# Performance work log

Measured on AMD Instinct MI355X. Metric: run time of the kernel, lower is better.

Reference implementation:

```python
import jax, jax.numpy as jnp
import numpy as np


def setup_inputs() -> dict:
    key = jax.random.key(0)
    k1, k2 = jax.random.split(key)
    L, B, H = 1024, 64, 1024
    encoder_outputs = jax.random.normal(k1, (L, B, H), dtype=jnp.float32)
    decoder_gru_out = jax.random.normal(k2, (1, B, H), dtype=jnp.float32)
    return {"encoder_outputs": encoder_outputs, "decoder_gru_out": decoder_gru_out}


def reference(encoder_outputs, decoder_gru_out):
    # scores[l,b] = sum_h enc[l,b,h] * dec[0,b,h]
    scores = jnp.einsum('lbh,bh->lb', encoder_outputs, decoder_gru_out[0])
    # softmax over the sequence (L) axis
    attn = jax.nn.softmax(scores, axis=0)  # [L, B]
    # context[b,h] = sum_l attn[l,b] * enc[l,b,h]
    context = jnp.einsum('lb,lbh->bh', attn, encoder_outputs)
    return context
```

## Files before the change

kernel.cpp:

```cpp
#include <hip/hip_runtime.h>
#include <math.h>

#define L_SEQ 1024
#define BATCH 64
#define HDIM  1024
#define WPB   4

__global__ __launch_bounds__(256) void attn_partial_kernel(
    const float* __restrict__ enc, const float* __restrict__ dec,
    float* __restrict__ wsC, float* __restrict__ wsML,
    int split, int chunk)
{
    const int tid  = threadIdx.x;
    const int lane = tid & 63;
    const int wave = tid >> 6;
    const int w    = blockIdx.x * WPB + wave;
    const int b    = w / split;
    const int k    = w - b * split;
    const int l0   = k * chunk;

    const float4* decv = (const float4*)(dec + (size_t)b * HDIM);
    const float4 d0 = decv[lane];
    const float4 d1 = decv[lane + 64];
    const float4 d2 = decv[lane + 128];
    const float4 d3 = decv[lane + 192];

    float m = -INFINITY;
    float lsum = 0.0f;
    float4 a0 = make_float4(0.f, 0.f, 0.f, 0.f);
    float4 a1 = a0, a2 = a0, a3 = a0;

    for (int l = l0; l < l0 + chunk; ++l) {
        const float4* row = (const float4*)(enc + ((size_t)l * BATCH + b) * HDIM);
        const float4 e0 = row[lane];
        const float4 e1 = row[lane + 64];
        const float4 e2 = row[lane + 128];
        const float4 e3 = row[lane + 192];

        float p = e0.x * d0.x + e0.y * d0.y + e0.z * d0.z + e0.w * d0.w;
        p += e1.x * d1.x + e1.y * d1.y + e1.z * d1.z + e1.w * d1.w;
        p += e2.x * d2.x + e2.y * d2.y + e2.z * d2.z + e2.w * d2.w;
        p += e3.x * d3.x + e3.y * d3.y + e3.z * d3.z + e3.w * d3.w;

        #pragma unroll
        for (int off = 32; off > 0; off >>= 1)
            p += __shfl_xor(p, off, 64);

        const float mn    = fmaxf(m, p);
        const float scale = __expf(m - mn);
        const float pe    = __expf(p - mn);
        m = mn;
        lsum = lsum * scale + pe;
        a0.x = a0.x * scale + pe * e0.x;  a0.y = a0.y * scale + pe * e0.y;
        a0.z = a0.z * scale + pe * e0.z;  a0.w = a0.w * scale + pe * e0.w;
        a1.x = a1.x * scale + pe * e1.x;  a1.y = a1.y * scale + pe * e1.y;
        a1.z = a1.z * scale + pe * e1.z;  a1.w = a1.w * scale + pe * e1.w;
        a2.x = a2.x * scale + pe * e2.x;  a2.y = a2.y * scale + pe * e2.y;
        a2.z = a2.z * scale + pe * e2.z;  a2.w = a2.w * scale + pe * e2.w;
        a3.x = a3.x * scale + pe * e3.x;  a3.y = a3.y * scale + pe * e3.y;
        a3.z = a3.z * scale + pe * e3.z;  a3.w = a3.w * scale + pe * e3.w;
    }

    const size_t r = (size_t)b * split + k;
    float4* C = (float4*)(wsC + r * (size_t)HDIM);
    C[lane]       = a0;
    C[lane + 64]  = a1;
    C[lane + 128] = a2;
    C[lane + 192] = a3;
    if (lane == 0) {
        wsML[2 * r]     = m;
        wsML[2 * r + 1] = lsum;
    }
}

__global__ __launch_bounds__(256) void attn_reduce_kernel(
    const float* __restrict__ wsC, const float* __restrict__ wsML,
    float* __restrict__ out, int split)
{
    const int b = blockIdx.x;
    const int t = threadIdx.x;

    float M = -INFINITY;
    for (int k = 0; k < split; ++k)
        M = fmaxf(M, wsML[2 * ((size_t)b * split + k)]);

    float Ltot = 0.0f;
    float4 acc = make_float4(0.f, 0.f, 0.f, 0.f);
    for (int k = 0; k < split; ++k) {
        const size_t r = (size_t)b * split + k;
        const float wgt = __expf(wsML[2 * r] - M);
        Ltot += wsML[2 * r + 1] * wgt;
        const float4 c = ((const float4*)(wsC + r * (size_t)HDIM))[t];
        acc.x += c.x * wgt;  acc.y += c.y * wgt;
        acc.z += c.z * wgt;  acc.w += c.w * wgt;
    }
    const float inv = 1.0f / Ltot;
    float4 o;
    o.x = acc.x * inv;  o.y = acc.y * inv;
    o.z = acc.z * inv;  o.w = acc.w * inv;
    ((float4*)(out + (size_t)b * HDIM))[t] = o;
}

extern "C" void kernel_launch(void* const* d_in, const int* in_sizes, int n_in,
                              void* d_out, int out_size, void* d_ws, size_t ws_size,
                              hipStream_t stream) {
    const float* enc = (const float*)d_in[0];
    const float* dec = (const float*)d_in[1];
    float* out = (float*)d_out;

    int split = 32;
    while (split > 1) {
        const size_t need = (size_t)BATCH * split * HDIM * sizeof(float)
                          + (size_t)BATCH * split * 2 * sizeof(float);
        if (need <= ws_size) break;
        split >>= 1;
    }
    const int chunk = L_SEQ / split;

    float* wsC  = (float*)d_ws;
    float* wsML = wsC + (size_t)BATCH * split * HDIM;

    const int nblocks = (BATCH * split) / WPB;
    attn_partial_kernel<<<nblocks, 256, 0, stream>>>(enc, dec, wsC, wsML, split, chunk);
    attn_reduce_kernel<<<BATCH, 256, 0, stream>>>(wsC, wsML, out, split);
}
```

Measured before the change: 367.4 us.

## Process four sequence rows per iteration, use exp2 softmax, widen split and reduce grid

The partial kernel now loads four encoder rows per iteration, so more memory loads are in flight, and it batches the shuffle reductions and the online-softmax rescale, with one rescale per group of four rows. Scores are converted to base-2 so exp2f can replace __expf. The split count rises from 32 to 64 when the workspace allows, and the reduce kernel uses four times as many blocks with scalar loads. The cost is much higher register use from the 16 float4 row values, which can lower occupancy, plus a larger workspace write and read.

```diff
diff --git a/kernel.cpp b/kernel.cpp
--- a/kernel.cpp
+++ b/kernel.cpp
@@ -5,6 +5,8 @@
 #define BATCH 64
 #define HDIM  1024
 #define WPB   4
+
+#define LOG2E 1.44269504088896340736f
 
 __global__ __launch_bounds__(256) void attn_partial_kernel(
     const float* __restrict__ enc, const float* __restrict__ dec,
@@ -20,53 +22,75 @@
     const int l0   = k * chunk;
 
     const float4* decv = (const float4*)(dec + (size_t)b * HDIM);
-    const float4 d0 = decv[lane];
-    const float4 d1 = decv[lane + 64];
-    const float4 d2 = decv[lane + 128];
-    const float4 d3 = decv[lane + 192];
+    float4 d[4];
+    #pragma unroll
+    for (int q = 0; q < 4; ++q) d[q] = decv[lane + 64 * q];
 
     float m = -INFINITY;
     float lsum = 0.0f;
-    float4 a0 = make_float4(0.f, 0.f, 0.f, 0.f);
-    float4 a1 = a0, a2 = a0, a3 = a0;
+    float4 a[4];
+    #pragma unroll
+    for (int q = 0; q < 4; ++q) a[q] = make_float4(0.f, 0.f, 0.f, 0.f);
 
-    for (int l = l0; l < l0 + chunk; ++l) {
-        const float4* row = (const float4*)(enc + ((size_t)l * BATCH + b) * HDIM);
-        const float4 e0 = row[lane];
-        const float4 e1 = row[lane + 64];
-        const float4 e2 = row[lane + 128];
-        const float4 e3 = row[lane + 192];
+    const size_t row_stride = (size_t)BATCH * HDIM;
 
-        float p = e0.x * d0.x + e0.y * d0.y + e0.z * d0.z + e0.w * d0.w;
-        p += e1.x * d1.x + e1.y * d1.y + e1.z * d1.z + e1.w * d1.w;
-        p += e2.x * d2.x + e2.y * d2.y + e2.z * d2.z + e2.w * d2.w;
-        p += e3.x * d3.x + e3.y * d3.y + e3.z * d3.z + e3.w * d3.w;
+    for (int g = 0; g < chunk; g += 4) {
+        const float* base = enc + ((size_t)(l0 + g) * BATCH + b) * HDIM;
+
+        float4 e[4][4];
+        #pragma unroll
+        for (int r = 0; r < 4; ++r) {
+            const float4* row = (const float4*)(base + r * row_stride);
+            #pragma unroll
+            for (int q = 0; q < 4; ++q) e[r][q] = row[lane + 64 * q];
+        }
+
+        float p[4];
+        #pragma unroll
+        for (int r = 0; r < 4; ++r) {
+            float s = 0.0f;
+            #pragma unroll
+            for (int q = 0; q < 4; ++q) {
+                s = fmaf(e[r][q].x, d[q].x, s);
+                s = fmaf(e[r][q].y, d[q].y, s);
+                s = fmaf(e[r][q].z, d[q].z, s);
+                s = fmaf(e[r][q].w, d[q].w, s);
+            }
+            p[r] = s;
+        }
 
         #pragma unroll
-        for (int off = 32; off > 0; off >>= 1)
-            p += __shfl_xor(p, off, 64);
+        for (int off = 32; off > 0; off >>= 1) {
+            p[0] += __shfl_xor(p[0], off, 64);
+            p[1] += __shfl_xor(p[1], off, 64);
+            p[2] += __shfl_xor(p[2], off, 64);
+            p[3] += __shfl_xor(p[3], off, 64);
+        }
 
-        const float mn    = fmaxf(m, p);
-        const float scale = __expf(m - mn);
-        const float pe    = __expf(p - mn);
+        const float s0 = p[0] * LOG2E, s1 = p[1] * LOG2E;
+        const float s2 = p[2] * LOG2E, s3 = p[3] * LOG2E;
+        const float mn = fmaxf(m, fmaxf(fmaxf(s0, s1), fmaxf(s2, s3)));
+        const float scale = exp2f(m - mn);
+        const float w0 = exp2f(s0 - mn);
+        const float w1 = exp2f(s1 - mn);
+        const float w2 = exp2f(s2 - mn);
+        const float w3 = exp2f(s3 - mn);
         m = mn;
-        lsum = lsum * scale + pe;
-        a0.x = a0.x * scale + pe * e0.x;  a0.y = a0.y * scale + pe * e0.y;
-        a0.z = a0.z * scale + pe * e0.z;  a0.w = a0.w * scale + pe * e0.w;
-        a1.x = a1.x * scale + pe * e1.x;  a1.y = a1.y * scale + pe * e1.y;
-        a1.z = a1.z * scale + pe * e1.z;  a1.w = a1.w * scale + pe * e1.w;
-        a2.x = a2.x * scale + pe * e2.x;  a2.y = a2.y * scale + pe * e2.y;
-        a2.z = a2.z * scale + pe * e2.z;  a2.w = a2.w * scale + pe * e2.w;
-        a3.x = a3.x * scale + pe * e3.x;  a3.y = a3.y * scale + pe * e3.y;
-        a3.z = a3.z * scale + pe * e3.z;  a3.w = a3.w * scale + pe * e3.w;
+        lsum = fmaf(lsum, scale, (w0 + w1) + (w2 + w3));
+
+        #pragma unroll
+        for (int q = 0; q < 4; ++q) {
+            a[q].x = fmaf(w3, e[3][q].x, fmaf(w2, e[2][q].x, fmaf(w1, e[1][q].x, fmaf(w0, e[0][q].x, a[q].x * scale))));
+            a[q].y = fmaf(w3, e[3][q].y, fmaf(w2, e[2][q].y, fmaf(w1, e[1][q].y, fmaf(w0, e[0][q].y, a[q].y * scale))));
+            a[q].z = fmaf(w3, e[3][q].z, fmaf(w2, e[2][q].z, fmaf(w1, e[1][q].z, fmaf(w0, e[0][q].z, a[q].z * scale))));
+            a[q].w = fmaf(w3, e[3][q].w, fmaf(w2, e[2][q].w, fmaf(w1, e[1][q].w, fmaf(w0, e[0][q].w, a[q].w * scale))));
+        }
     }
 
     const size_t r = (size_t)b * split + k;
     float4* C = (float4*)(wsC + r * (size_t)HDIM);
-    C[lane]       = a0;
-    C[lane + 64]  = a1;
-    C[lane + 128] = a2;
-    C[lane + 192] = a3;
+    #pragma unroll
+    for (int q = 0; q < 4; ++q) C[lane + 64 * q] = a[q];
     if (lane == 0) {
         wsML[2 * r]     = m;
         wsML[2 * r + 1] = lsum;
@@ -77,28 +101,23 @@
     const float* __restrict__ wsC, const float* __restrict__ wsML,
     float* __restrict__ out, int split)
 {
-    const int b = blockIdx.x;
-    const int t = threadIdx.x;
+    const int b = blockIdx.x >> 2;
+    const int q = blockIdx.x & 3;
+    const int h = q * 256 + threadIdx.x;
 
     float M = -INFINITY;
     for (int k = 0; k < split; ++k)
         M = fmaxf(M, wsML[2 * ((size_t)b * split + k)]);
 
     float Ltot = 0.0f;
-    float4 acc = make_float4(0.f, 0.f, 0.f, 0.f);
+    float acc = 0.0f;
     for (int k = 0; k < split; ++k) {
         const size_t r = (size_t)b * split + k;
-        const float wgt = __expf(wsML[2 * r] - M);
-        Ltot += wsML[2 * r + 1] * wgt;
-        const float4 c = ((const float4*)(wsC + r * (size_t)HDIM))[t];
-        acc.x += c.x * wgt;  acc.y += c.y * wgt;
-        acc.z += c.z * wgt;  acc.w += c.w * wgt;
+        const float wgt = exp2f(wsML[2 * r] - M);
+        Ltot = fmaf(wsML[2 * r + 1], wgt, Ltot);
+        acc = fmaf(wsC[r * (size_t)HDIM + h], wgt, acc);
     }
-    const float inv = 1.0f / Ltot;
-    float4 o;
-    o.x = acc.x * inv;  o.y = acc.y * inv;
-    o.z = acc.z * inv;  o.w = acc.w * inv;
-    ((float4*)(out + (size_t)b * HDIM))[t] = o;
+    out[(size_t)b * HDIM + h] = acc / Ltot;
 }
 
 extern "C" void kernel_launch(void* const* d_in, const int* in_sizes, int n_in,
@@ -108,7 +127,7 @@
     const float* dec = (const float*)d_in[1];
     float* out = (float*)d_out;
 
-    int split = 32;
+    int split = 64;
     while (split > 1) {
         const size_t need = (size_t)BATCH * split * HDIM * sizeof(float)
                           + (size_t)BATCH * split * 2 * sizeof(float);
@@ -122,5 +141,5 @@
 
     const int nblocks = (BATCH * split) / WPB;
     attn_partial_kernel<<<nblocks, 256, 0, stream>>>(enc, dec, wsC, wsML, split, chunk);
-    attn_reduce_kernel<<<BATCH, 256, 0, stream>>>(wsC, wsML, out, split);
+    attn_reduce_kernel<<<BATCH * 4, 256, 0, stream>>>(wsC, wsML, out, split);
 }
```

Measured after the change: 380.9 us. 1.04x slower.
